# Performance work log

Hardware: AMD Instinct MI355X
Metric: run time of the kernel (lower is better)

## Reference

```python
import jax, jax.numpy as jnp
import numpy as np

N_NODES = 20000
N_EDGES = 160000
N_GRAPHS = 64
IN_DIM = 128
HID = 512
N_CLASSES = 16


def setup_inputs() -> dict:
    key = jax.random.key(0)
    ks = jax.random.split(key, 16)
    x = jax.random.normal(ks[0], (N_NODES, IN_DIM), jnp.float32)
    src = jax.random.randint(ks[1], (N_EDGES,), 0, N_NODES, jnp.int32)
    dst = jax.random.randint(ks[2], (N_EDGES,), 0, N_NODES, jnp.int32)
    graph_ids = jnp.sort(jax.random.randint(ks[3], (N_NODES,), 0, N_GRAPHS, jnp.int32))

    def glorot(k, shape):
        lim = float(np.sqrt(6.0 / (shape[0] + shape[1])))
        return jax.random.uniform(k, shape, jnp.float32, -lim, lim)

    return {
        "x": x, "src": src, "dst": dst, "graph_ids": graph_ids,
        "W1": glorot(ks[4], (IN_DIM, HID)), "b1": jnp.zeros((HID,), jnp.float32),
        "W2": glorot(ks[5], (HID, HID)), "b2": jnp.zeros((HID,), jnp.float32),
        "W3": glorot(ks[6], (HID, HID)), "b3": jnp.zeros((HID,), jnp.float32),
        "Wc1": glorot(ks[7], (HID, HID)), "bc1": jnp.zeros((HID,), jnp.float32),
        "Wc2": glorot(ks[8], (HID, HID)), "bc2": jnp.zeros((HID,), jnp.float32),
        "Wc3": glorot(ks[9], (HID, N_CLASSES)), "bc3": jnp.zeros((N_CLASSES,), jnp.float32),
    }


def _graph_conv(h, W, b, src, dst, dout_isqrt, din_isqrt):
    # DGL GraphConv, norm='both': h' = D_in^{-1/2} A D_out^{-1/2} h W + b
    h = h * dout_isqrt[:, None]          # pre-normalize by sqrt(out-degree)
    h = h @ W                             # project first (cheaper than on edges)
    msg = h[src]                          # gather  [E, out]
    agg = jax.ops.segment_sum(msg, dst, num_segments=N_NODES)  # scatter-add
    return agg * din_isqrt[:, None] + b   # post-normalize by sqrt(in-degree)


def reference(x, src, dst, graph_ids, W1, b1, W2, b2, W3, b3,
              Wc1, bc1, Wc2, bc2, Wc3, bc3):
    ones_e = jnp.ones((N_EDGES,), jnp.float32)
    deg_out = jax.ops.segment_sum(ones_e, src, num_segments=N_NODES)
    deg_in = jax.ops.segment_sum(ones_e, dst, num_segments=N_NODES)
    dout_isqrt = jax.lax.rsqrt(jnp.clip(deg_out, 1.0))
    din_isqrt = jax.lax.rsqrt(jnp.clip(deg_in, 1.0))

    h = jax.nn.relu(_graph_conv(x, W1, b1, src, dst, dout_isqrt, din_isqrt))
    h = jax.nn.relu(_graph_conv(h, W2, b2, src, dst, dout_isqrt, din_isqrt))
    h = jax.nn.relu(_graph_conv(h, W3, b3, src, dst, dout_isqrt, din_isqrt))

    # dgl.mean_nodes: per-graph mean pooling
    sums = jax.ops.segment_sum(h, graph_ids, num_segments=N_GRAPHS)
    counts = jax.ops.segment_sum(jnp.ones((N_NODES,), jnp.float32), graph_ids,
                                 num_segments=N_GRAPHS)
    hg = sums / jnp.clip(counts, 1.0)[:, None]   # [G, HID]

    out = jax.nn.relu(hg @ Wc1 + bc1)
    out = jax.nn.relu(out @ Wc2 + bc2)
    return out @ Wc3 + bc3                       # [G, n_classes]
```

## Files before the change

kernel.cpp:

```cpp
#include <hip/hip_runtime.h>

#define N_NODES 20000
#define N_EDGES 160000
#define N_GRAPHS 64
#define IN_DIM 128
#define HID 512
#define N_CLASSES 16

#define POISON_I ((int)0xAAAAAAAA)

#define DEGCAP 40

typedef unsigned short u16;
typedef short bf16x8 __attribute__((ext_vector_type(8)));
typedef float f32x4 __attribute__((ext_vector_type(4)));

__device__ __forceinline__ u16 bf16_rn(float x) {
  unsigned u = __float_as_uint(x);
  unsigned r = u + 0x7FFFu + ((u >> 16) & 1u);
  return (u16)(r >> 16);
}

__device__ __forceinline__ void addh(float* a, int h) {
  a[0] += __uint_as_float((unsigned)h << 16);
  a[1] += __uint_as_float((unsigned)h & 0xFFFF0000u);
}

#define DEG_BLOCKS ((N_EDGES + 255) / 256)
#define TT_BLOCKS 144
__global__ void prep(const int* __restrict__ src, const int* __restrict__ dst,
                     int* __restrict__ dout,
                     int* __restrict__ cursor, int* __restrict__ bucket,
                     const float* __restrict__ W1, const float* __restrict__ W2,
                     const float* __restrict__ W3,
                     u16* __restrict__ w1h, u16* __restrict__ w2h,
                     u16* __restrict__ w3h) {
  __shared__ u16 tile[64][65];
  if (blockIdx.x < DEG_BLOCKS) {
    const int e = blockIdx.x * 256 + threadIdx.x;
    if (e < N_EDGES) {
      const int s = src[e];
      const int d = dst[e];
      atomicAdd(dout + s, 1);
      const int pos = atomicAdd(cursor + d, 1) - POISON_I;
      if (pos < DEGCAP) bucket[d * DEGCAP + pos] = s;
    }
    return;
  }
  const int b = blockIdx.x - DEG_BLOCKS;
  const float* W; u16* th; int K, k0, n0;
  if (b < 16)      { W = W1; th = w1h; K = IN_DIM; k0 = (b & 1) * 64;        n0 = (b >> 1) * 64; }
  else if (b < 80) { W = W2; th = w2h; K = HID;    k0 = ((b - 16) & 7) * 64; n0 = ((b - 16) >> 3) * 64; }
  else             { W = W3; th = w3h; K = HID;    k0 = ((b - 80) & 7) * 64; n0 = ((b - 80) >> 3) * 64; }
  const int t = threadIdx.x;
  const int tn = t & 63;
  const int tk4 = t >> 6;
#pragma unroll
  for (int pass = 0; pass < 16; pass++) {
    const int k = pass * 4 + tk4;
    tile[tn][k] = bf16_rn(W[(size_t)(k0 + k) * HID + n0 + tn]);
  }
  __syncthreads();
#pragma unroll
  for (int pass = 0; pass < 16; pass++) {
    const int n = pass * 4 + tk4;
    th[(size_t)(n0 + n) * K + k0 + tn] = tile[n][tn];
  }
}

__global__ __launch_bounds__(256) void norms(const int* __restrict__ dout,
                                             const int* __restrict__ din,
                                             float* __restrict__ dosq,
                                             float* __restrict__ disq,
                                             const int* __restrict__ gid,
                                             int* __restrict__ gstart) {
  const int i = blockIdx.x * 256 + threadIdx.x;
  if (i >= N_NODES) return;
  dosq[i] = rsqrtf(fmaxf((float)(dout[i] - POISON_I), 1.0f));
  disq[i] = rsqrtf(fmaxf((float)(din[i] - POISON_I), 1.0f));
  const int g = gid[i];
  const int gp = (i == 0) ? -1 : gid[i - 1];
  for (int k = gp + 1; k <= g; k++) gstart[k] = i;
  if (i == N_NODES - 1) {
    for (int k = g + 1; k <= N_GRAPHS; k++) gstart[k] = N_NODES;
  }
}

__global__ __launch_bounds__(256) void gather_f32(
    const float* __restrict__ x, const int* __restrict__ din,
    const int* __restrict__ bucket, const float* __restrict__ dosq,
    const float* __restrict__ disq, u16* __restrict__ gh) {
  const int node = blockIdx.x * 8 + (threadIdx.x >> 5);
  if (node >= N_NODES) return;
  const int lane4 = (threadIdx.x & 31) * 4;

  int cnt = din[node] - POISON_I;
  if (cnt > DEGCAP) cnt = DEGCAP;
  const int beg = node * DEGCAP;
  const int end = beg + cnt;

  float4 acc = make_float4(0.f, 0.f, 0.f, 0.f);
  int e = beg;
  for (; e + 8 <= end; e += 8) {
    int s[8];
#pragma unroll
    for (int q = 0; q < 8; q++) s[q] = bucket[e + q];
    float4 v[8];
    float dd[8];
#pragma unroll
    for (int q = 0; q < 8; q++) {
      dd[q] = dosq[s[q]];
      v[q] = *(const float4*)(x + (size_t)s[q] * IN_DIM + lane4);
    }
#pragma unroll
    for (int q = 0; q < 8; q++) {
      acc.x += dd[q] * v[q].x; acc.y += dd[q] * v[q].y;
      acc.z += dd[q] * v[q].z; acc.w += dd[q] * v[q].w;
    }
  }
  for (; e < end; e++) {
    const int s0 = bucket[e];
    const float d0 = dosq[s0];
    const float4 v0 = *(const float4*)(x + (size_t)s0 * IN_DIM + lane4);
    acc.x += d0 * v0.x; acc.y += d0 * v0.y; acc.z += d0 * v0.z; acc.w += d0 * v0.w;
  }
  const float di = disq[node];
  ushort4 vh;
  vh.x = bf16_rn(acc.x * di);
  vh.y = bf16_rn(acc.y * di);
  vh.z = bf16_rn(acc.z * di);
  vh.w = bf16_rn(acc.w * di);
  *(ushort4*)(gh + (size_t)node * IN_DIM + lane4) = vh;
}

__global__ __launch_bounds__(256) void gather_hi(
    const u16* __restrict__ hin, const int* __restrict__ din,
    const int* __restrict__ bucket, const float* __restrict__ disq,
    u16* __restrict__ gh) {
  const int node = blockIdx.x * 4 + (threadIdx.x >> 6);
  if (node >= N_NODES) return;
  const int c8 = (threadIdx.x & 63) * 8;
  const u16* base = hin + c8;

  int cnt = din[node] - POISON_I;
  if (cnt > DEGCAP) cnt = DEGCAP;
  const int beg = node * DEGCAP;
  const int end = beg + cnt;

  float acc[8] = {};
  int e = beg;
  for (; e + 8 <= end; e += 8) {
    int s[8];
#pragma unroll
    for (int q = 0; q < 8; q++) s[q] = bucket[e + q];
    int4 h[8];
#pragma unroll
    for (int q = 0; q < 8; q++) h[q] = *(const int4*)(base + (size_t)s[q] * HID);
#pragma unroll
    for (int q = 0; q < 8; q++) {
      addh(acc + 0, h[q].x); addh(acc + 2, h[q].y);
      addh(acc + 4, h[q].z); addh(acc + 6, h[q].w);
    }
  }
  for (; e + 4 <= end; e += 4) {
    const int s0 = bucket[e], s1 = bucket[e + 1], s2 = bucket[e + 2], s3 = bucket[e + 3];
    const int4 h0 = *(const int4*)(base + (size_t)s0 * HID);
    const int4 h1 = *(const int4*)(base + (size_t)s1 * HID);
    const int4 h2 = *(const int4*)(base + (size_t)s2 * HID);
    const int4 h3 = *(const int4*)(base + (size_t)s3 * HID);
    addh(acc + 0, h0.x); addh(acc + 2, h0.y); addh(acc + 4, h0.z); addh(acc + 6, h0.w);
    addh(acc + 0, h1.x); addh(acc + 2, h1.y); addh(acc + 4, h1.z); addh(acc + 6, h1.w);
    addh(acc + 0, h2.x); addh(acc + 2, h2.y); addh(acc + 4, h2.z); addh(acc + 6, h2.w);
    addh(acc + 0, h3.x); addh(acc + 2, h3.y); addh(acc + 4, h3.z); addh(acc + 6, h3.w);
  }
  for (; e < end; e++) {
    const int4 h0 = *(const int4*)(base + (size_t)bucket[e] * HID);
    addh(acc + 0, h0.x); addh(acc + 2, h0.y); addh(acc + 4, h0.z); addh(acc + 6, h0.w);
  }

  const float di = disq[node];
  int4 hi;
  int* hp = (int*)&hi;
#pragma unroll
  for (int i = 0; i < 4; i++) {
    const u16 h0 = bf16_rn(acc[2 * i] * di);
    const u16 h1 = bf16_rn(acc[2 * i + 1] * di);
    hp[i] = (int)h0 | ((int)h1 << 16);
  }
  *(int4*)(gh + (size_t)node * HID + c8) = hi;
}

#define GBK 32
#define LROW 40
template <int POOL>
__global__ __launch_bounds__(256) void gemm_mfma(
    const u16* __restrict__ Ah, int lda,
    const u16* __restrict__ Bh,
    const float* __restrict__ bias, const float* __restrict__ dosq,
    u16* __restrict__ Cb,
    const int* __restrict__ gid, float* __restrict__ hgp,
    int M, int K) {
  __shared__ u16 sAh[2][128 * LROW];
  __shared__ u16 sBh[2][128 * LROW];

  const int n = blockIdx.x;
  const int r = (n & 7) + (n >> 5) * 8;
  const int c = (n >> 3) & 3;
  const int row0 = r * 128;
  const int col0 = c * 128;
  if (row0 >= M) return;

  const int t = threadIdx.x;
  const int lane = t & 63;
  const int wav  = t >> 6;
  const int wr = (wav >> 1) * 64;
  const int wc = (wav & 1) * 64;
  const int fm = lane & 15;
  const int fq = lane >> 4;

  const int r0 = t >> 2;
  const int u0 = t & 3;

  const int arow0 = row0 + r0;
  const int arow1 = row0 + r0 + 64;
  const size_t aoff0 = (size_t)((arow0 < M) ? arow0 : 0) * lda + u0 * 8;
  const size_t aoff1 = (size_t)((arow1 < M) ? arow1 : 0) * lda + u0 * 8;
  const size_t boff0 = (size_t)(col0 + r0) * K + u0 * 8;
  const size_t boff1 = (size_t)(col0 + r0 + 64) * K + u0 * 8;
  const int ldso0 = r0 * LROW + u0 * 8;
  const int ldso1 = (r0 + 64) * LROW + u0 * 8;

  f32x4 acc[4][4] = {};

  {
    const int4 va0 = *(const int4*)(Ah + aoff0);
    const int4 va1 = *(const int4*)(Ah + aoff1);
    const int4 vb0 = *(const int4*)(Bh + boff0);
    const int4 vb1 = *(const int4*)(Bh + boff1);
    *(int4*)(sAh[0] + ldso0) = va0;
    *(int4*)(sAh[0] + ldso1) = va1;
    *(int4*)(sBh[0] + ldso0) = vb0;
    *(int4*)(sBh[0] + ldso1) = vb1;
  }
  __syncthreads();

  int cur = 0;
  for (int k0 = 0; k0 < K; k0 += GBK) {
    const bool has_next = (k0 + GBK) < K;
    int4 va0, va1, vb0, vb1;
    if (has_next) {
      const int kn = k0 + GBK;
      va0 = *(const int4*)(Ah + aoff0 + kn);
      va1 = *(const int4*)(Ah + aoff1 + kn);
      vb0 = *(const int4*)(Bh + boff0 + kn);
      vb1 = *(const int4*)(Bh + boff1 + kn);
    }

    bf16x8 fah[4], fbh[4];
#pragma unroll
    for (int i = 0; i < 4; i++) {
      fah[i] = *(const bf16x8*)(sAh[cur] + (wr + i * 16 + fm) * LROW + fq * 8);
      fbh[i] = *(const bf16x8*)(sBh[cur] + (wc + i * 16 + fm) * LROW + fq * 8);
    }
#pragma unroll
    for (int j = 0; j < 4; j++)
#pragma unroll
      for (int i = 0; i < 4; i++)
        acc[i][j] = __builtin_amdgcn_mfma_f32_16x16x32_bf16(fah[i], fbh[j], acc[i][j], 0, 0, 0);

    if (has_next) {
      *(int4*)(sAh[cur ^ 1] + ldso0) = va0;
      *(int4*)(sAh[cur ^ 1] + ldso1) = va1;
      *(int4*)(sBh[cur ^ 1] + ldso0) = vb0;
      *(int4*)(sBh[cur ^ 1] + ldso1) = vb1;
    }
    __syncthreads();
    cur ^= 1;
  }

  if (POOL == 0) {
#pragma unroll
    for (int i = 0; i < 4; i++) {
#pragma unroll
      for (int rr = 0; rr < 4; rr++) {
        const int grow = row0 + wr + i * 16 + fq * 4 + rr;
        if (grow < M) {
          const float dsc = dosq[grow];
#pragma unroll
          for (int j = 0; j < 4; j++) {
            const int gcol = col0 + wc + j * 16 + fm;
            const float v = fmaxf(acc[i][j][rr] + bias[gcol], 0.0f) * dsc;
            Cb[(size_t)grow * HID + gcol] = bf16_rn(v);
          }
        }
      }
    }
  } else {
    float* pool = (float*)sAh;
    const int g0 = gid[row0];
    const int rl = (row0 + 127 < M) ? row0 + 127 : M - 1;
    const int gspan = gid[rl] - g0 + 1;
    if (gspan <= 8) {
      for (int i = t; i < gspan * 128; i += 256) pool[i] = 0.f;
      __syncthreads();
#pragma unroll
      for (int j = 0; j < 4; j++) {
        const int lcol = wc + j * 16 + fm;
        const float bv = bias[col0 + lcol];
        float run = 0.f;
        int cur2 = -1;
#pragma unroll
        for (int i = 0; i < 4; i++)
#pragma unroll
          for (int rr = 0; rr < 4; rr++) {
            const int grow = row0 + wr + i * 16 + fq * 4 + rr;
            if (grow < M) {
              const int sg = gid[grow] - g0;
              const float v = fmaxf(acc[i][j][rr] + bv, 0.0f);
              if (sg != cur2) {
                if (cur2 >= 0) atomicAdd(pool + cur2 * 128 + lcol, run);
                run = 0.f;
                cur2 = sg;
              }
              run += v;
            }
          }
        if (cur2 >= 0) atomicAdd(pool + cur2 * 128 + lcol, run);
      }
      __syncthreads();
      for (int i = t; i < gspan * 128; i += 256)
        atomicAdd(hgp + (size_t)(g0 + (i >> 7)) * HID + col0 + (i & 127), pool[i]);
    } else {
#pragma unroll
      for (int j = 0; j < 4; j++) {
        const int lcol = wc + j * 16 + fm;
        const float bv = bias[col0 + lcol];
        float run = 0.f;
        int cur2 = -1;
#pragma unroll
        for (int i = 0; i < 4; i++)
#pragma unroll
          for (int rr = 0; rr < 4; rr++) {
            const int grow = row0 + wr + i * 16 + fq * 4 + rr;
            if (grow < M) {
              const int sg = gid[grow];
              const float v = fmaxf(acc[i][j][rr] + bv, 0.0f);
              if (sg != cur2) {
                if (cur2 >= 0) atomicAdd(hgp + (size_t)cur2 * HID + col0 + lcol, run);
                run = 0.f;
                cur2 = sg;
              }
              run += v;
            }
          }
        if (cur2 >= 0) atomicAdd(hgp + (size_t)cur2 * HID + col0 + lcol, run);
      }
    }
  }
}

__global__ __launch_bounds__(1024) void mlp_fused(
    const float* __restrict__ hgp, const int* __restrict__ gstart,
    const float* __restrict__ Wc1, const float* __restrict__ bc1,
    const float* __restrict__ Wc2, const float* __restrict__ bc2,
    const float* __restrict__ Wc3, const float* __restrict__ bc3,
    float* __restrict__ out) {
  __shared__ float sA[HID];
  __shared__ float sB[HID];
  __shared__ float4 red4[8][128];
  float* red = (float*)red4;

  const int g = blockIdx.x;
  const int t = threadIdx.x;
  const int cg = t & 127;
  const int sl = t >> 7;

  if (t < HID) {
    const float inv = 1.0f / fmaxf((float)(gstart[g + 1] - gstart[g]), 1.0f);
    sA[t] = hgp[(size_t)g * HID + t] * inv;
  }
  __syncthreads();

  {
    float4 a = make_float4(0.f, 0.f, 0.f, 0.f);
    const int kb = sl * 64;
#pragma unroll 8
    for (int k = kb; k < kb + 64; k++) {
      const float s = sA[k];
      const float4 w = *(const float4*)(Wc1 + (size_t)k * HID + cg * 4);
      a.x += s * w.x; a.y += s * w.y; a.z += s * w.z; a.w += s * w.w;
    }
    red4[sl][cg] = a;
  }
  __syncthreads();
  if (sl == 0) {
    float4 a = red4[0][cg];
#pragma unroll
    for (int s = 1; s < 8; s++) {
      const float4 b = red4[s][cg];
      a.x += b.x; a.y += b.y; a.z += b.z; a.w += b.w;
    }
    const float4 b = *(const float4*)(bc1 + cg * 4);
    sB[cg * 4 + 0] = fmaxf(a.x + b.x, 0.f);
    sB[cg * 4 + 1] = fmaxf(a.y + b.y, 0.f);
    sB[cg * 4 + 2] = fmaxf(a.z + b.z, 0.f);
    sB[cg * 4 + 3] = fmaxf(a.w + b.w, 0.f);
  }
  __syncthreads();

  {
    float4 a = make_float4(0.f, 0.f, 0.f, 0.f);
    const int kb = sl * 64;
#pragma unroll 8
    for (int k = kb; k < kb + 64; k++) {
      const float s = sB[k];
      const float4 w = *(const float4*)(Wc2 + (size_t)k * HID + cg * 4);
      a.x += s * w.x; a.y += s * w.y; a.z += s * w.z; a.w += s * w.w;
    }
    red4[sl][cg] = a;
  }
  __syncthreads();
  if (sl == 0) {
    float4 a = red4[0][cg];
#pragma unroll
    for (int s = 1; s < 8; s++) {
      const float4 b = red4[s][cg];
      a.x += b.x; a.y += b.y; a.z += b.z; a.w += b.w;
    }
    const float4 b = *(const float4*)(bc2 + cg * 4);
    sA[cg * 4 + 0] = fmaxf(a.x + b.x, 0.f);
    sA[cg * 4 + 1] = fmaxf(a.y + b.y, 0.f);
    sA[cg * 4 + 2] = fmaxf(a.z + b.z, 0.f);
    sA[cg * 4 + 3] = fmaxf(a.w + b.w, 0.f);
  }
  __syncthreads();

  {
    const int col = t & 15;
    const int s3 = t >> 4;
    float a = 0.f;
#pragma unroll 8
    for (int k = s3; k < HID; k += 64) a += sA[k] * Wc3[(size_t)k * N_CLASSES + col];
    red[t] = a;
  }
  __syncthreads();
#pragma unroll
  for (int off = 512; off >= 16; off >>= 1) {
    if (t < off) red[t] += red[t + off];
    __syncthreads();
  }
  if (t < 16) out[(size_t)g * N_CLASSES + t] = red[t] + bc3[t];
}

extern "C" void kernel_launch(void* const* d_in, const int* in_sizes, int n_in,
                              void* d_out, int out_size, void* d_ws, size_t ws_size,
                              hipStream_t stream) {
  const float* x   = (const float*)d_in[0];
  const int*   src = (const int*)d_in[1];
  const int*   dst = (const int*)d_in[2];
  const int*   gid = (const int*)d_in[3];
  const float* W1  = (const float*)d_in[4];  const float* b1  = (const float*)d_in[5];
  const float* W2  = (const float*)d_in[6];  const float* b2  = (const float*)d_in[7];
  const float* W3  = (const float*)d_in[8];  const float* b3  = (const float*)d_in[9];
  const float* Wc1 = (const float*)d_in[10]; const float* bc1 = (const float*)d_in[11];
  const float* Wc2 = (const float*)d_in[12]; const float* bc2 = (const float*)d_in[13];
  const float* Wc3 = (const float*)d_in[14]; const float* bc3 = (const float*)d_in[15];
  float* out = (float*)d_out;

  char* p = (char*)d_ws;
  u16* gA = (u16*)p;                  p += (size_t)N_NODES * HID * 2;
  u16* hB = (u16*)p;                  p += (size_t)N_NODES * HID * 2;
  u16* w1h = (u16*)p;                 p += (size_t)HID * IN_DIM * 2;
  u16* w2h = (u16*)p;                 p += (size_t)HID * HID * 2;
  u16* w3h = (u16*)p;                 p += (size_t)HID * HID * 2;
  float* dosq = (float*)p;            p += N_NODES * 4;
  float* disq = (float*)p;            p += N_NODES * 4;
  float* hgp = (float*)p;             p += (size_t)N_GRAPHS * HID * 4;
  int* deg_out_i = (int*)p;           p += N_NODES * 4;
  int* cursor    = (int*)p;           p += N_NODES * 4;
  int* gstart    = (int*)p;           p += (N_GRAPHS + 1) * 4;
  int* bucket    = (int*)p;           p += (size_t)N_NODES * DEGCAP * 4;

  prep<<<DEG_BLOCKS + TT_BLOCKS, 256, 0, stream>>>(
      src, dst, deg_out_i, cursor, bucket, W1, W2, W3, w1h, w2h, w3h);
  norms<<<(N_NODES + 255) / 256, 256, 0, stream>>>(deg_out_i, cursor, dosq, disq, gid, gstart);

  const int ggrid = 640;
  const int gat_blocks = (N_NODES + 3) / 4;

  gather_f32<<<(N_NODES + 7) / 8, 256, 0, stream>>>(x, cursor, bucket, dosq, disq, gA);
  gemm_mfma<0><<<ggrid, 256, 0, stream>>>(gA, IN_DIM, w1h, b1, dosq, hB, gid, hgp, N_NODES, IN_DIM);

  gather_hi<<<gat_blocks, 256, 0, stream>>>(hB, cursor, bucket, disq, gA);
  gemm_mfma<0><<<ggrid, 256, 0, stream>>>(gA, HID, w2h, b2, dosq, hB, gid, hgp, N_NODES, HID);

  gather_hi<<<gat_blocks, 256, 0, stream>>>(hB, cursor, bucket, disq, gA);
  gemm_mfma<1><<<ggrid, 256, 0, stream>>>(gA, HID, w3h, b3, dosq, nullptr, gid, hgp, N_NODES, HID);

  mlp_fused<<<N_GRAPHS, 1024, 0, stream>>>(hgp, gstart, Wc1, bc1, Wc2, bc2, Wc3, bc3, out);
}
```

Before: 252.8 us.

## Keep weight slice resident in LDS, persistent row loop, drop norms kernel

The GEMM now loads the whole 128-column weight slice into shared memory once per block and loops persistently over row tiles (256 blocks), reading A fragments directly from global memory instead of double-buffering through LDS. The separate norms kernel is removed: degree rsqrt factors are computed inline from raw counts, and the per-graph node count is found by binary search in the MLP kernel. This cuts one launch and repeated weight staging, but loses LDS staging of A (uncoalesced-ish fragment loads) and K=512 needs about 130KB of LDS, which limits occupancy.

Result: slower. 310.9 us (+23.0%).

```diff
diff --git a/kernel.cpp b/kernel.cpp
--- a/kernel.cpp
+++ b/kernel.cpp
@@ -24,6 +24,10 @@
 __device__ __forceinline__ void addh(float* a, int h) {
   a[0] += __uint_as_float((unsigned)h << 16);
   a[1] += __uint_as_float((unsigned)h & 0xFFFF0000u);
+}
+
+__device__ __forceinline__ float deg_isq(int raw) {
+  return rsqrtf(fmaxf((float)(raw - POISON_I), 1.0f));
 }
 
 #define DEG_BLOCKS ((N_EDGES + 255) / 256)
@@ -68,34 +72,16 @@
   }
 }
 
-__global__ __launch_bounds__(256) void norms(const int* __restrict__ dout,
-                                             const int* __restrict__ din,
-                                             float* __restrict__ dosq,
-                                             float* __restrict__ disq,
-                                             const int* __restrict__ gid,
-                                             int* __restrict__ gstart) {
-  const int i = blockIdx.x * 256 + threadIdx.x;
-  if (i >= N_NODES) return;
-  dosq[i] = rsqrtf(fmaxf((float)(dout[i] - POISON_I), 1.0f));
-  disq[i] = rsqrtf(fmaxf((float)(din[i] - POISON_I), 1.0f));
-  const int g = gid[i];
-  const int gp = (i == 0) ? -1 : gid[i - 1];
-  for (int k = gp + 1; k <= g; k++) gstart[k] = i;
-  if (i == N_NODES - 1) {
-    for (int k = g + 1; k <= N_GRAPHS; k++) gstart[k] = N_NODES;
-  }
-}
-
 __global__ __launch_bounds__(256) void gather_f32(
     const float* __restrict__ x, const int* __restrict__ din,
-    const int* __restrict__ bucket, const float* __restrict__ dosq,
-    const float* __restrict__ disq, u16* __restrict__ gh) {
+    const int* __restrict__ bucket, const int* __restrict__ dout,
+    u16* __restrict__ gh) {
   const int node = blockIdx.x * 8 + (threadIdx.x >> 5);
   if (node >= N_NODES) return;
   const int lane4 = (threadIdx.x & 31) * 4;
 
-  int cnt = din[node] - POISON_I;
-  if (cnt > DEGCAP) cnt = DEGCAP;
+  const int rawc = din[node] - POISON_I;
+  const int cnt = (rawc > DEGCAP) ? DEGCAP : rawc;
   const int beg = node * DEGCAP;
   const int end = beg + cnt;
 
@@ -109,7 +95,7 @@
     float dd[8];
 #pragma unroll
     for (int q = 0; q < 8; q++) {
-      dd[q] = dosq[s[q]];
+      dd[q] = deg_isq(dout[s[q]]);
       v[q] = *(const float4*)(x + (size_t)s[q] * IN_DIM + lane4);
     }
 #pragma unroll
@@ -120,11 +106,11 @@
   }
   for (; e < end; e++) {
     const int s0 = bucket[e];
-    const float d0 = dosq[s0];
+    const float d0 = deg_isq(dout[s0]);
     const float4 v0 = *(const float4*)(x + (size_t)s0 * IN_DIM + lane4);
     acc.x += d0 * v0.x; acc.y += d0 * v0.y; acc.z += d0 * v0.z; acc.w += d0 * v0.w;
   }
-  const float di = disq[node];
+  const float di = rsqrtf(fmaxf((float)rawc, 1.0f));
   ushort4 vh;
   vh.x = bf16_rn(acc.x * di);
   vh.y = bf16_rn(acc.y * di);
@@ -135,15 +121,14 @@
 
 __global__ __launch_bounds__(256) void gather_hi(
     const u16* __restrict__ hin, const int* __restrict__ din,
-    const int* __restrict__ bucket, const float* __restrict__ disq,
-    u16* __restrict__ gh) {
+    const int* __restrict__ bucket, u16* __restrict__ gh) {
   const int node = blockIdx.x * 4 + (threadIdx.x >> 6);
   if (node >= N_NODES) return;
   const int c8 = (threadIdx.x & 63) * 8;
   const u16* base = hin + c8;
 
-  int cnt = din[node] - POISON_I;
-  if (cnt > DEGCAP) cnt = DEGCAP;
+  const int rawc = din[node] - POISON_I;
+  const int cnt = (rawc > DEGCAP) ? DEGCAP : rawc;
   const int beg = node * DEGCAP;
   const int end = beg + cnt;
 
@@ -178,7 +163,7 @@
     addh(acc + 0, h0.x); addh(acc + 2, h0.y); addh(acc + 4, h0.z); addh(acc + 6, h0.w);
   }
 
-  const float di = disq[node];
+  const float di = rsqrtf(fmaxf((float)rawc, 1.0f));
   int4 hi;
   int* hp = (int*)&hi;
 #pragma unroll
@@ -190,27 +175,35 @@
   *(int4*)(gh + (size_t)node * HID + c8) = hi;
 }
 
-#define GBK 32
-#define LROW 40
-template <int POOL>
+template <int POOL, int K>
 __global__ __launch_bounds__(256) void gemm_mfma(
-    const u16* __restrict__ Ah, int lda,
+    const u16* __restrict__ Ah,
     const u16* __restrict__ Bh,
-    const float* __restrict__ bias, const float* __restrict__ dosq,
+    const float* __restrict__ bias, const int* __restrict__ dout,
     u16* __restrict__ Cb,
     const int* __restrict__ gid, float* __restrict__ hgp,
-    int M, int K) {
-  __shared__ u16 sAh[2][128 * LROW];
-  __shared__ u16 sBh[2][128 * LROW];
-
-  const int n = blockIdx.x;
-  const int r = (n & 7) + (n >> 5) * 8;
-  const int c = (n >> 3) & 3;
-  const int row0 = r * 128;
+    int M) {
+  constexpr int LROWB = K + 8;
+  __shared__ u16 sB[128 * LROWB];
+  __shared__ float pool[POOL ? 8 * 128 : 1];
+
+  const int c = blockIdx.x & 3;
+  const int rg = blockIdx.x >> 2;
   const int col0 = c * 128;
-  if (row0 >= M) return;
-
   const int t = threadIdx.x;
+
+  {
+    constexpr int KI4 = K / 8;
+    constexpr int NI4 = 128 * KI4;
+    const u16* Bsl = Bh + (size_t)col0 * K;
+    for (int i = t; i < NI4; i += 256) {
+      const int n = i / KI4;
+      const int kk = i - n * KI4;
+      *(int4*)(sB + n * LROWB + kk * 8) = *(const int4*)(Bsl + (size_t)i * 8);
+    }
+  }
+  __syncthreads();
+
   const int lane = t & 63;
   const int wav  = t >> 6;
   const int wr = (wav >> 1) * 64;
@@ -218,149 +211,117 @@
   const int fm = lane & 15;
   const int fq = lane >> 4;
 
-  const int r0 = t >> 2;
-  const int u0 = t & 3;
-
-  const int arow0 = row0 + r0;
-  const int arow1 = row0 + r0 + 64;
-  const size_t aoff0 = (size_t)((arow0 < M) ? arow0 : 0) * lda + u0 * 8;
-  const size_t aoff1 = (size_t)((arow1 < M) ? arow1 : 0) * lda + u0 * 8;
-  const size_t boff0 = (size_t)(col0 + r0) * K + u0 * 8;
-  const size_t boff1 = (size_t)(col0 + r0 + 64) * K + u0 * 8;
-  const int ldso0 = r0 * LROW + u0 * 8;
-  const int ldso1 = (r0 + 64) * LROW + u0 * 8;
-
-  f32x4 acc[4][4] = {};
-
-  {
-    const int4 va0 = *(const int4*)(Ah + aoff0);
-    const int4 va1 = *(const int4*)(Ah + aoff1);
-    const int4 vb0 = *(const int4*)(Bh + boff0);
-    const int4 vb1 = *(const int4*)(Bh + boff1);
-    *(int4*)(sAh[0] + ldso0) = va0;
-    *(int4*)(sAh[0] + ldso1) = va1;
-    *(int4*)(sBh[0] + ldso0) = vb0;
-    *(int4*)(sBh[0] + ldso1) = vb1;
-  }
-  __syncthreads();
-
-  int cur = 0;
-  for (int k0 = 0; k0 < K; k0 += GBK) {
-    const bool has_next = (k0 + GBK) < K;
-    int4 va0, va1, vb0, vb1;
-    if (has_next) {
-      const int kn = k0 + GBK;
-      va0 = *(const int4*)(Ah + aoff0 + kn);
-      va1 = *(const int4*)(Ah + aoff1 + kn);
-      vb0 = *(const int4*)(Bh + boff0 + kn);
-      vb1 = *(const int4*)(Bh + boff1 + kn);
-    }
-
-    bf16x8 fah[4], fbh[4];
+  const int NT = (M + 127) / 128;
+  for (int r = rg; r < NT; r += 64) {
+    const int row0 = r * 128;
+
+    size_t aoff[4];
 #pragma unroll
     for (int i = 0; i < 4; i++) {
-      fah[i] = *(const bf16x8*)(sAh[cur] + (wr + i * 16 + fm) * LROW + fq * 8);
-      fbh[i] = *(const bf16x8*)(sBh[cur] + (wc + i * 16 + fm) * LROW + fq * 8);
-    }
-#pragma unroll
-    for (int j = 0; j < 4; j++)
+      const int ar = row0 + wr + i * 16 + fm;
+      aoff[i] = (size_t)((ar < M) ? ar : 0) * K + fq * 8;
+    }
+
+    f32x4 acc[4][4] = {};
+#pragma unroll 4
+    for (int k0 = 0; k0 < K; k0 += 32) {
+      bf16x8 fah[4], fbh[4];
 #pragma unroll
       for (int i = 0; i < 4; i++)
-        acc[i][j] = __builtin_amdgcn_mfma_f32_16x16x32_bf16(fah[i], fbh[j], acc[i][j], 0, 0, 0);
-
-    if (has_next) {
-      *(int4*)(sAh[cur ^ 1] + ldso0) = va0;
-      *(int4*)(sAh[cur ^ 1] + ldso1) = va1;
-      *(int4*)(sBh[cur ^ 1] + ldso0) = vb0;
-      *(int4*)(sBh[cur ^ 1] + ldso1) = vb1;
-    }
-    __syncthreads();
-    cur ^= 1;
-  }
-
-  if (POOL == 0) {
-#pragma unroll
-    for (int i = 0; i < 4; i++) {
-#pragma unroll
-      for (int rr = 0; rr < 4; rr++) {
-        const int grow = row0 + wr + i * 16 + fq * 4 + rr;
-        if (grow < M) {
-          const float dsc = dosq[grow];
-#pragma unroll
-          for (int j = 0; j < 4; j++) {
-            const int gcol = col0 + wc + j * 16 + fm;
-            const float v = fmaxf(acc[i][j][rr] + bias[gcol], 0.0f) * dsc;
-            Cb[(size_t)grow * HID + gcol] = bf16_rn(v);
+        fah[i] = *(const bf16x8*)(Ah + aoff[i] + k0);
+#pragma unroll
+      for (int j = 0; j < 4; j++)
+        fbh[j] = *(const bf16x8*)(sB + (wc + j * 16 + fm) * LROWB + k0 + fq * 8);
+#pragma unroll
+      for (int j = 0; j < 4; j++)
+#pragma unroll
+        for (int i = 0; i < 4; i++)
+          acc[i][j] = __builtin_amdgcn_mfma_f32_16x16x32_bf16(fah[i], fbh[j], acc[i][j], 0, 0, 0);
+    }
+
+    if (POOL == 0) {
+#pragma unroll
+      for (int i = 0; i < 4; i++) {
+#pragma unroll
+        for (int rr = 0; rr < 4; rr++) {
+          const int grow = row0 + wr + i * 16 + fq * 4 + rr;
+          if (grow < M) {
+            const float dsc = deg_isq(dout[grow]);
+#pragma unroll
+            for (int j = 0; j < 4; j++) {
+              const int gcol = col0 + wc + j * 16 + fm;
+              const float v = fmaxf(acc[i][j][rr] + bias[gcol], 0.0f) * dsc;
+              Cb[(size_t)grow * HID + gcol] = bf16_rn(v);
+            }
           }
         }
       }
-    }
-  } else {
-    float* pool = (float*)sAh;
-    const int g0 = gid[row0];
-    const int rl = (row0 + 127 < M) ? row0 + 127 : M - 1;
-    const int gspan = gid[rl] - g0 + 1;
-    if (gspan <= 8) {
-      for (int i = t; i < gspan * 128; i += 256) pool[i] = 0.f;
-      __syncthreads();
-#pragma unroll
-      for (int j = 0; j < 4; j++) {
-        const int lcol = wc + j * 16 + fm;
-        const float bv = bias[col0 + lcol];
-        float run = 0.f;
-        int cur2 = -1;
-#pragma unroll
-        for (int i = 0; i < 4; i++)
-#pragma unroll
-          for (int rr = 0; rr < 4; rr++) {
-            const int grow = row0 + wr + i * 16 + fq * 4 + rr;
-            if (grow < M) {
-              const int sg = gid[grow] - g0;
-              const float v = fmaxf(acc[i][j][rr] + bv, 0.0f);
-              if (sg != cur2) {
-                if (cur2 >= 0) atomicAdd(pool + cur2 * 128 + lcol, run);
-                run = 0.f;
-                cur2 = sg;
+    } else {
+      const int g0 = gid[row0];
+      const int rl = (row0 + 127 < M) ? row0 + 127 : M - 1;
+      const int gspan = gid[rl] - g0 + 1;
+      if (gspan <= 8) {
+        for (int i = t; i < gspan * 128; i += 256) pool[i] = 0.f;
+        __syncthreads();
+#pragma unroll
+        for (int j = 0; j < 4; j++) {
+          const int lcol = wc + j * 16 + fm;
+          const float bv = bias[col0 + lcol];
+          float run = 0.f;
+          int cur = -1;
+#pragma unroll
+          for (int i = 0; i < 4; i++)
+#pragma unroll
+            for (int rr = 0; rr < 4; rr++) {
+              const int grow = row0 + wr + i * 16 + fq * 4 + rr;
+              if (grow < M) {
+                const int sg = gid[grow] - g0;
+                const float v = fmaxf(acc[i][j][rr] + bv, 0.0f);
+                if (sg != cur) {
+                  if (cur >= 0) atomicAdd(pool + cur * 128 + lcol, run);
+                  run = 0.f;
+                  cur = sg;
+                }
+                run += v;
               }
-              run += v;
             }
-          }
-        if (cur2 >= 0) atomicAdd(pool + cur2 * 128 + lcol, run);
+          if (cur >= 0) atomicAdd(pool + cur * 128 + lcol, run);
+        }
+        __syncthreads();
+        for (int i = t; i < gspan * 128; i += 256)
+          atomicAdd(hgp + (size_t)(g0 + (i >> 7)) * HID + col0 + (i & 127), pool[i]);
+      } else {
+#pragma unroll
+        for (int j = 0; j < 4; j++) {
+          const int lcol = wc + j * 16 + fm;
+          const float bv = bias[col0 + lcol];
+          float run = 0.f;
+          int cur = -1;
+#pragma unroll
+          for (int i = 0; i < 4; i++)
+#pragma unroll
+            for (int rr = 0; rr < 4; rr++) {
+              const int grow = row0 + wr + i * 16 + fq * 4 + rr;
+              if (grow < M) {
+                const int sg = gid[grow];
+                const float v = fmaxf(acc[i][j][rr] + bv, 0.0f);
+                if (sg != cur) {
+                  if (cur >= 0) atomicAdd(hgp + (size_t)cur * HID + col0 + lcol, run);
+                  run = 0.f;
+                  cur = sg;
+                }
+                run += v;
+              }
+            }
+          if (cur >= 0) atomicAdd(hgp + (size_t)cur * HID + col0 + lcol, run);
+        }
       }
-      __syncthreads();
-      for (int i = t; i < gspan * 128; i += 256)
-        atomicAdd(hgp + (size_t)(g0 + (i >> 7)) * HID + col0 + (i & 127), pool[i]);
-    } else {
-#pragma unroll
-      for (int j = 0; j < 4; j++) {
-        const int lcol = wc + j * 16 + fm;
-        const float bv = bias[col0 + lcol];
-        float run = 0.f;
-        int cur2 = -1;
-#pragma unroll
-        for (int i = 0; i < 4; i++)
-#pragma unroll
-          for (int rr = 0; rr < 4; rr++) {
-            const int grow = row0 + wr + i * 16 + fq * 4 + rr;
-            if (grow < M) {
-              const int sg = gid[grow];
-              const float v = fmaxf(acc[i][j][rr] + bv, 0.0f);
-              if (sg != cur2) {
-                if (cur2 >= 0) atomicAdd(hgp + (size_t)cur2 * HID + col0 + lcol, run);
-                run = 0.f;
-                cur2 = sg;
-              }
-              run += v;
-            }
-          }
-        if (cur2 >= 0) atomicAdd(hgp + (size_t)cur2 * HID + col0 + lcol, run);
-      }
     }
   }
 }
 
 __global__ __launch_bounds__(1024) void mlp_fused(
-    const float* __restrict__ hgp, const int* __restrict__ gstart,
+    const float* __restrict__ hgp, const int* __restrict__ gid,
     const float* __restrict__ Wc1, const float* __restrict__ bc1,
     const float* __restrict__ Wc2, const float* __restrict__ bc2,
     const float* __restrict__ Wc3, const float* __restrict__ bc3,
@@ -368,6 +329,7 @@
   __shared__ float sA[HID];
   __shared__ float sB[HID];
   __shared__ float4 red4[8][128];
+  __shared__ int scount;
   float* red = (float*)red4;
 
   const int g = blockIdx.x;
@@ -375,11 +337,16 @@
   const int cg = t & 127;
   const int sl = t >> 7;
 
-  if (t < HID) {
-    const float inv = 1.0f / fmaxf((float)(gstart[g + 1] - gstart[g]), 1.0f);
-    sA[t] = hgp[(size_t)g * HID + t] * inv;
-  }
-  __syncthreads();
+  if (t == 0) {
+    int lo = 0, hi = N_NODES;
+    while (lo < hi) { const int mid = (lo + hi) >> 1; if (gid[mid] < g) lo = mid + 1; else hi = mid; }
+    int lo2 = lo, hi2 = N_NODES;
+    while (lo2 < hi2) { const int mid = (lo2 + hi2) >> 1; if (gid[mid] < g + 1) lo2 = mid + 1; else hi2 = mid; }
+    scount = lo2 - lo;
+  }
+  if (t < HID) sA[t] = hgp[(size_t)g * HID + t];
+  __syncthreads();
+  const float inv = 1.0f / fmaxf((float)scount, 1.0f);
 
   {
     float4 a = make_float4(0.f, 0.f, 0.f, 0.f);
@@ -401,10 +368,10 @@
       a.x += b.x; a.y += b.y; a.z += b.z; a.w += b.w;
     }
     const float4 b = *(const float4*)(bc1 + cg * 4);
-    sB[cg * 4 + 0] = fmaxf(a.x + b.x, 0.f);
-    sB[cg * 4 + 1] = fmaxf(a.y + b.y, 0.f);
-    sB[cg * 4 + 2] = fmaxf(a.z + b.z, 0.f);
-    sB[cg * 4 + 3] = fmaxf(a.w + b.w, 0.f);
+    sB[cg * 4 + 0] = fmaxf(a.x * inv + b.x, 0.f);
+    sB[cg * 4 + 1] = fmaxf(a.y * inv + b.y, 0.f);
+    sB[cg * 4 + 2] = fmaxf(a.z * inv + b.z, 0.f);
+    sB[cg * 4 + 3] = fmaxf(a.w * inv + b.w, 0.f);
   }
   __syncthreads();
 
@@ -473,29 +440,25 @@
   u16* w1h = (u16*)p;                 p += (size_t)HID * IN_DIM * 2;
   u16* w2h = (u16*)p;                 p += (size_t)HID * HID * 2;
   u16* w3h = (u16*)p;                 p += (size_t)HID * HID * 2;
-  float* dosq = (float*)p;            p += N_NODES * 4;
-  float* disq = (float*)p;            p += N_NODES * 4;
   float* hgp = (float*)p;             p += (size_t)N_GRAPHS * HID * 4;
   int* deg_out_i = (int*)p;           p += N_NODES * 4;
   int* cursor    = (int*)p;           p += N_NODES * 4;
-  int* gstart    = (int*)p;           p += (N_GRAPHS + 1) * 4;
   int* bucket    = (int*)p;           p += (size_t)N_NODES * DEGCAP * 4;
 
   prep<<<DEG_BLOCKS + TT_BLOCKS, 256, 0, stream>>>(
       src, dst, deg_out_i, cursor, bucket, W1, W2, W3, w1h, w2h, w3h);
-  norms<<<(N_NODES + 255) / 256, 256, 0, stream>>>(deg_out_i, cursor, dosq, disq, gid, gstart);
-
-  const int ggrid = 640;
+
+  const int ggrid = 256;
   const int gat_blocks = (N_NODES + 3) / 4;
 
-  gather_f32<<<(N_NODES + 7) / 8, 256, 0, stream>>>(x, cursor, bucket, dosq, disq, gA);
-  gemm_mfma<0><<<ggrid, 256, 0, stream>>>(gA, IN_DIM, w1h, b1, dosq, hB, gid, hgp, N_NODES, IN_DIM);
-
-  gather_hi<<<gat_blocks, 256, 0, stream>>>(hB, cursor, bucket, disq, gA);
-  gemm_mfma<0><<<ggrid, 256, 0, stream>>>(gA, HID, w2h, b2, dosq, hB, gid, hgp, N_NODES, HID);
-
-  gather_hi<<<gat_blocks, 256, 0, stream>>>(hB, cursor, bucket, disq, gA);
-  gemm_mfma<1><<<ggrid, 256, 0, stream>>>(gA, HID, w3h, b3, dosq, nullptr, gid, hgp, N_NODES, HID);
-
-  mlp_fused<<<N_GRAPHS, 1024, 0, stream>>>(hgp, gstart, Wc1, bc1, Wc2, bc2, Wc3, bc3, out);
-}
+  gather_f32<<<(N_NODES + 7) / 8, 256, 0, stream>>>(x, cursor, bucket, deg_out_i, gA);
+  gemm_mfma<0, IN_DIM><<<ggrid, 256, 0, stream>>>(gA, w1h, b1, deg_out_i, hB, gid, hgp, N_NODES);
+
+  gather_hi<<<gat_blocks, 256, 0, stream>>>(hB, cursor, bucket, gA);
+  gemm_mfma<0, HID><<<ggrid, 256, 0, stream>>>(gA, w2h, b2, deg_out_i, hB, gid, hgp, N_NODES);
+
+  gather_hi<<<gat_blocks, 256, 0, stream>>>(hB, cursor, bucket, gA);
+  gemm_mfma<1, HID><<<ggrid, 256, 0, stream>>>(gA, w3h, b3, deg_out_i, nullptr, gid, hgp, N_NODES);
+
+  mlp_fused<<<N_GRAPHS, 1024, 0, stream>>>(hgp, gid, Wc1, bc1, Wc2, bc2, Wc3, bc3, out);
+}
```
